# Optimization experiments

Hardware: AMD Instinct MI355X
Metric: run time of the kernel (lower is better)

The kernel has to match this reference:

```python
import jax, jax.numpy as jnp
import numpy as np

DIM = 1024
NUM_HEADS = 16
DPH = DIM // NUM_HEADS
B, S = 4, 2048
LN_EPS = 1e-5


def layer_norm(x, g, b):
    mu = jnp.mean(x, axis=-1, keepdims=True)
    var = jnp.mean((x - mu) ** 2, axis=-1, keepdims=True)
    return (x - mu) * jax.lax.rsqrt(var + LN_EPS) * g + b


def setup_inputs() -> dict:
    key = jax.random.key(0)
    ks = jax.random.split(key, 10)
    sd = 0.02
    return {
        "x": jax.random.normal(ks[0], (B, S, DIM), dtype=jnp.float32),
        "Wq": jax.random.normal(ks[1], (DIM, DIM), dtype=jnp.float32) * sd,
        "Wk": jax.random.normal(ks[2], (DIM, DIM), dtype=jnp.float32) * sd,
        "Wv": jax.random.normal(ks[3], (DIM, DIM), dtype=jnp.float32) * sd,
        "bq": jnp.zeros((DIM,), dtype=jnp.float32),
        "bk": jnp.zeros((DIM,), dtype=jnp.float32),
        "bv": jnp.zeros((DIM,), dtype=jnp.float32),
        "ln1_g": jnp.ones((DIM,), dtype=jnp.float32),
        "ln1_b": jnp.zeros((DIM,), dtype=jnp.float32),
        "W1": jax.random.normal(ks[4], (DIM, 4 * DIM), dtype=jnp.float32) * sd,
        "b1": jnp.zeros((4 * DIM,), dtype=jnp.float32),
        "W2": jax.random.normal(ks[5], (4 * DIM, DIM), dtype=jnp.float32) * sd,
        "b2": jnp.zeros((DIM,), dtype=jnp.float32),
        "ln2_g": jnp.ones((DIM,), dtype=jnp.float32),
        "ln2_b": jnp.zeros((DIM,), dtype=jnp.float32),
    }


def reference(x, Wq, Wk, Wv, bq, bk, bv, ln1_g, ln1_b, W1, b1, W2, b2, ln2_g, ln2_b):
    b, s, d = x.shape
    # QKV projections (heads are independent linears -> one fused GEMM each)
    q = (x @ Wq + bq).reshape(b, s, NUM_HEADS, DPH)
    k = (x @ Wk + bk).reshape(b, s, NUM_HEADS, DPH)
    v = (x @ Wv + bv).reshape(b, s, NUM_HEADS, DPH)
    # Faithful quirk: module scales by 1/sqrt(dph) twice => 1/dph total
    scores = jnp.einsum("bqhd,bkhd->bhqk", q, k) / DPH
    causal = jnp.tril(jnp.ones((s, s), dtype=bool))
    scores = jnp.where(causal, scores, -1e9)
    attn = jax.nn.softmax(scores, axis=-1)
    out_attn = jnp.einsum("bhqk,bkhd->bqhd", attn, v).reshape(b, s, d)
    # Add & Norm 1 (no output projection in original)
    h = layer_norm(out_attn + x, ln1_g, ln1_b)
    # Feed-forward (dropout is identity at eval)
    ffn = jax.nn.relu(h @ W1 + b1) @ W2 + b2
    # Add & Norm 2
    return layer_norm(ffn + h, ln2_g, ln2_b)
```

## Files before the change

### kernel.cpp

```cpp
#include <hip/hip_runtime.h>
#include <hip/hip_bf16.h>

typedef __bf16 bf16_t;
typedef __bf16 bf16x8 __attribute__((ext_vector_type(8)));
typedef __bf16 bf16x4 __attribute__((ext_vector_type(4)));
typedef float  floatx4 __attribute__((ext_vector_type(4)));

#define DIM    1024
#define S_LEN  2048
#define NHEAD  16

template <typename T>
__device__ __forceinline__ bf16x8 load8bf(const T* src) {
  if constexpr (sizeof(T) == 2) {
    return *reinterpret_cast<const bf16x8*>(src);
  } else {
    floatx4 f0 = *reinterpret_cast<const floatx4*>(src);
    floatx4 f1 = *reinterpret_cast<const floatx4*>(src + 4);
    bf16x8 h;
    h[0] = (bf16_t)f0[0]; h[1] = (bf16_t)f0[1];
    h[2] = (bf16_t)f0[2]; h[3] = (bf16_t)f0[3];
    h[4] = (bf16_t)f1[0]; h[5] = (bf16_t)f1[1];
    h[6] = (bf16_t)f1[2]; h[7] = (bf16_t)f1[3];
    return h;
  }
}

__device__ __forceinline__ void gll16(const bf16_t* g, bf16_t* l) {
  __builtin_amdgcn_global_load_lds(
      (const __attribute__((address_space(1))) void*)g,
      (__attribute__((address_space(3))) void*)l, 16, 0, 0);
}

__device__ __forceinline__ void xcd_remap(int& bx, int& by, int& bz) {
  const int gx = gridDim.x, gy = gridDim.y, gz = gridDim.z;
  const int nwg = gx * gy * gz;
  int lin = ((int)blockIdx.z * gy + blockIdx.y) * gx + blockIdx.x;
  int cid = lin;
  if ((nwg & 7) == 0) cid = (lin & 7) * (nwg >> 3) + (lin >> 3);
  bx = cid % gx;
  int t = cid / gx;
  bz = t % gz;
  by = t / gz;
}

__global__ __launch_bounds__(256) void conv_bf(const float* __restrict__ in,
                                               bf16_t* __restrict__ out) {
  size_t i = ((size_t)blockIdx.x * 256 + threadIdx.x) * 8;
  *reinterpret_cast<bf16x8*>(out + i) = load8bf(in + i);
}

__global__ __launch_bounds__(256) void convT3(
    const float* __restrict__ in0, int ldi0, bf16_t* __restrict__ out0,
    const float* __restrict__ in1, int ldi1, bf16_t* __restrict__ out1,
    const float* __restrict__ in2, int ldi2, bf16_t* __restrict__ out2,
    int ldo) {
  __shared__ bf16_t tile[32][33];
  const int z = blockIdx.z;
  const float* in = (z == 0) ? in0 : ((z == 1) ? in1 : in2);
  bf16_t* out = (z == 0) ? out0 : ((z == 1) ? out1 : out2);
  int ldi = (z == 0) ? ldi0 : ((z == 1) ? ldi1 : ldi2);
  int tx = threadIdx.x, ty = threadIdx.y;
  int n0 = blockIdx.x * 32, k0 = blockIdx.y * 32;
#pragma unroll
  for (int i = 0; i < 4; ++i)
    tile[ty + 8 * i][tx] = (bf16_t)in[(size_t)(k0 + ty + 8 * i) * ldi + n0 + tx];
  __syncthreads();
#pragma unroll
  for (int i = 0; i < 4; ++i)
    out[(size_t)(n0 + ty + 8 * i) * ldo + k0 + tx] = tile[tx][ty + 8 * i];
}

#define BM 128
#define BN 128
#define BK 32

template <typename TC>
__global__ __launch_bounds__(256) void gemm_abt(
    const bf16_t* __restrict__ A, int lda,
    const bf16_t* __restrict__ Bt, int zBRow,
    TC* __restrict__ C, int ldc, int zCOff,
    const float* __restrict__ bias0, const float* __restrict__ bias1,
    const float* __restrict__ bias2,
    int K, int relu, int accum) {
  __shared__ bf16_t As[2][BM * BK];
  __shared__ bf16_t Bs[2][BN * BK];

  int bx, by, bz;
  xcd_remap(bx, by, bz);
  const int z = bz;
  const float* bias = (z == 0) ? bias0 : ((z == 1) ? bias1 : bias2);
  const bf16_t* Bz = Bt + (size_t)z * zBRow * K;
  C += (size_t)z * zCOff;

  const int tid  = threadIdx.x;
  const int lane = tid & 63;
  const int wave = tid >> 6;
  const int wr   = wave >> 1;
  const int wc   = wave & 1;
  const int quad = lane >> 4;
  const int l15  = lane & 15;
  const int m0   = by * BM;
  const int n0   = bx * BN;
  const int swz = ((lane & 3) ^ ((lane >> 3) & 3)) * 8;
  const int rsw = (l15 >> 1) & 3;

  auto stageB = [&](int buf, int kt) {
#pragma unroll
    for (int i = 0; i < 2; ++i)
      gll16(Bz + (size_t)(n0 + wave * 32 + i * 16 + (lane >> 2)) * K +
                kt * BK + swz,
            &Bs[buf][(wave * 32 + i * 16) * BK]);
  };
  auto stageA = [&](int buf, int kt) {
#pragma unroll
    for (int i = 0; i < 2; ++i)
      gll16(A + (size_t)(m0 + wave * 32 + i * 16 + (lane >> 2)) * lda +
                kt * BK + swz,
            &As[buf][(wave * 32 + i * 16) * BK]);
  };

  floatx4 acc[4][4];
#pragma unroll
  for (int i = 0; i < 4; ++i)
#pragma unroll
    for (int j = 0; j < 4; ++j) acc[i][j] = (floatx4)(0.0f);

  const int kIters = K / BK;
  stageB(0, 0);
  stageA(0, 0);
  __syncthreads();

  int cur = 0;
  for (int kt = 0; kt < kIters; ++kt) {
    const int nxt = cur ^ 1;
    if (kt + 1 < kIters) {
      stageB(nxt, kt + 1);
      stageA(nxt, kt + 1);
    }

    bf16x8 a[4], b[4];
#pragma unroll
    for (int i = 0; i < 4; ++i)
      a[i] = *reinterpret_cast<const bf16x8*>(
          &As[cur][(wr * 64 + i * 16 + l15) * BK + (quad ^ rsw) * 8]);
#pragma unroll
    for (int j = 0; j < 4; ++j)
      b[j] = *reinterpret_cast<const bf16x8*>(
          &Bs[cur][(wc * 64 + j * 16 + l15) * BK + (quad ^ rsw) * 8]);
#pragma unroll
    for (int i = 0; i < 4; ++i)
#pragma unroll
      for (int j = 0; j < 4; ++j)
        acc[i][j] = __builtin_amdgcn_mfma_f32_16x16x32_bf16(a[i], b[j], acc[i][j], 0, 0, 0);

    __syncthreads();
    cur = nxt;
  }

#pragma unroll
  for (int j = 0; j < 4; ++j) {
    int gn = n0 + wc * 64 + j * 16 + l15;
    float bv = bias ? bias[gn] : 0.0f;
#pragma unroll
    for (int i = 0; i < 4; ++i) {
      int gm = m0 + wr * 64 + i * 16 + quad * 4;
#pragma unroll
      for (int r = 0; r < 4; ++r) {
        float v = acc[i][j][r] + bv;
        if (relu) v = fmaxf(v, 0.0f);
        size_t idx = (size_t)(gm + r) * ldc + gn;
        if (accum) v += (float)C[idx];
        C[idx] = (TC)v;
      }
    }
  }
}

__global__ __launch_bounds__(256) void transpose_v(const bf16_t* __restrict__ in,
                                                   bf16_t* __restrict__ outp) {
  __shared__ bf16_t tile[32][33];
  int tx = threadIdx.x, ty = threadIdx.y;
  int s0 = blockIdx.x * 32, d0 = blockIdx.y * 32, bh = blockIdx.z;
  int z = bh >> 4, h = bh & 15;
  const bf16_t* src = in + (size_t)z * S_LEN * 3072 + 2048 + h * 64;
#pragma unroll
  for (int i = 0; i < 4; ++i)
    tile[ty + 8 * i][tx] = src[(size_t)(s0 + ty + 8 * i) * 3072 + d0 + tx];
  __syncthreads();
  bf16_t* dst = outp + (size_t)bh * 64 * S_LEN;
#pragma unroll
  for (int i = 0; i < 4; ++i)
    dst[(size_t)(d0 + ty + 8 * i) * S_LEN + s0 + tx] = tile[tx][ty + 8 * i];
}

#define TQ  64
#define TK  64
#define AST 72
#define QSCALE 0.02254211f

struct KVregs { bf16x8 k[2]; bf16x8 v[2]; };

__global__ __launch_bounds__(256, 2) void attn_mfma2(
    const bf16_t* __restrict__ qkv, const bf16_t* __restrict__ vt,
    float* __restrict__ out) {
  __shared__ bf16_t QsPs[TQ * AST];
  __shared__ bf16_t Ks[TK * AST];
  __shared__ bf16_t Vs[TK * AST];

  const int tid  = threadIdx.x;
  const int lane = tid & 63;
  const int w    = tid >> 6;
  const int quad = lane >> 4;
  const int l15  = lane & 15;
  int pi, h, z;
  xcd_remap(pi, h, z);
  const int qb2[2] = {pi, 31 - pi};
  const bf16_t* qkv_b = qkv + (size_t)z * S_LEN * 3072;
  const bf16_t* vt_bh = vt + ((size_t)z * NHEAD + h) * 64 * S_LEN;
  float* out_b = out + (size_t)z * S_LEN * DIM;

  const int ktEnd = qb2[1] + 1;

  auto kv_load = [&](KVregs& r, int kt) {
#pragma unroll
    for (int p = 0; p < 2; ++p) {
      int id  = p * 256 + tid;
      int row = id >> 3;
      int c8  = (id & 7) * 8;
      r.k[p] = *reinterpret_cast<const bf16x8*>(
          qkv_b + (size_t)(kt * TK + row) * 3072 + 1024 + h * 64 + c8);
      r.v[p] = *reinterpret_cast<const bf16x8*>(
          vt_bh + (size_t)row * S_LEN + kt * TK + c8);
    }
  };
  auto kv_write = [&](KVregs& r) {
#pragma unroll
    for (int p = 0; p < 2; ++p) {
      int id  = p * 256 + tid;
      int row = id >> 3;
      int c8  = (id & 7) * 8;
      *reinterpret_cast<bf16x8*>(&Ks[row * AST + c8]) = r.k[p];
      *reinterpret_cast<bf16x8*>(&Vs[row * AST + c8]) = r.v[p];
    }
  };

  KVregs RA, RB;
  kv_load(RA, 0);

  bf16x8 aq[2][2];
  for (int tile = 0; tile < 2; ++tile) {
    if (tile) __syncthreads();
    const int qg0 = qb2[tile] * TQ;
#pragma unroll
    for (int p = 0; p < 2; ++p) {
      int id  = p * 256 + tid;
      int row = id >> 3;
      int c8  = (id & 7) * 8;
      bf16x8 v = *reinterpret_cast<const bf16x8*>(
          qkv_b + (size_t)(qg0 + row) * 3072 + h * 64 + c8);
      bf16x8 o;
#pragma unroll
      for (int e = 0; e < 8; ++e) o[e] = (bf16_t)((float)v[e] * QSCALE);
      *reinterpret_cast<bf16x8*>(&QsPs[row * AST + c8]) = o;
    }
    __syncthreads();
#pragma unroll
    for (int ks = 0; ks < 2; ++ks)
      aq[tile][ks] = *reinterpret_cast<const bf16x8*>(
          &QsPs[(w * 16 + l15) * AST + ks * 32 + quad * 8]);
  }

  float lp[2][4];
  floatx4 O[2][4];
#pragma unroll
  for (int t = 0; t < 2; ++t)
#pragma unroll
    for (int r = 0; r < 4; ++r) lp[t][r] = 0.0f;
#pragma unroll
  for (int t = 0; t < 2; ++t)
#pragma unroll
    for (int dt = 0; dt < 4; ++dt) O[t][dt] = (floatx4)(0.0f);

  auto step = [&](int kt, KVregs& cur, KVregs& nxt) {
    if (kt + 1 < ktEnd) kv_load(nxt, kt + 1);
    asm volatile("s_waitcnt lgkmcnt(0)" ::: "memory");
    __builtin_amdgcn_s_barrier();
    kv_write(cur);
    asm volatile("s_waitcnt lgkmcnt(0)" ::: "memory");
    __builtin_amdgcn_s_barrier();

    bf16x8 bk[4][2], bv[4][2];
#pragma unroll
    for (int i = 0; i < 4; ++i)
#pragma unroll
      for (int ks = 0; ks < 2; ++ks) {
        bk[i][ks] = *reinterpret_cast<const bf16x8*>(
            &Ks[(i * 16 + l15) * AST + ks * 32 + quad * 8]);
        bv[i][ks] = *reinterpret_cast<const bf16x8*>(
            &Vs[(i * 16 + l15) * AST + ks * 32 + quad * 8]);
      }

#pragma unroll
    for (int tile = 0; tile < 2; ++tile) {
      const int qtb = qb2[tile] * TQ + w * 16;
      if (kt * TK > qtb + 15) continue;

      floatx4 s[4];
      __builtin_amdgcn_s_setprio(1);
#pragma unroll
      for (int ktl = 0; ktl < 4; ++ktl) {
        s[ktl] = __builtin_amdgcn_mfma_f32_16x16x32_bf16(
            aq[tile][0], bk[ktl][0], (floatx4)(0.0f), 0, 0, 0);
        s[ktl] = __builtin_amdgcn_mfma_f32_16x16x32_bf16(
            aq[tile][1], bk[ktl][1], s[ktl], 0, 0, 0);
      }
      __builtin_amdgcn_s_setprio(0);
      if (kt * TK + TK - 1 > qtb) {
#pragma unroll
        for (int ktl = 0; ktl < 4; ++ktl) {
          int gk = kt * TK + ktl * 16 + l15;
#pragma unroll
          for (int r = 0; r < 4; ++r) {
            int gq = qtb + quad * 4 + r;
            if (gk > gq) s[ktl][r] = -1e30f;
          }
        }
      }
#pragma unroll
      for (int ktl = 0; ktl < 4; ++ktl)
#pragma unroll
        for (int r = 0; r < 4; ++r) {
          float p = exp2f(s[ktl][r]);
          lp[tile][r] += p;
          QsPs[(w * 16 + quad * 4 + r) * AST + ktl * 16 + l15] = (bf16_t)p;
        }

      bf16x8 ap0 = *reinterpret_cast<const bf16x8*>(
          &QsPs[(w * 16 + l15) * AST + quad * 8]);
      bf16x8 ap1 = *reinterpret_cast<const bf16x8*>(
          &QsPs[(w * 16 + l15) * AST + 32 + quad * 8]);
      __builtin_amdgcn_s_setprio(1);
#pragma unroll
      for (int dt = 0; dt < 4; ++dt) {
        O[tile][dt] = __builtin_amdgcn_mfma_f32_16x16x32_bf16(
            ap0, bv[dt][0], O[tile][dt], 0, 0, 0);
        O[tile][dt] = __builtin_amdgcn_mfma_f32_16x16x32_bf16(
            ap1, bv[dt][1], O[tile][dt], 0, 0, 0);
      }
      __builtin_amdgcn_s_setprio(0);
    }
  };

  for (int kt = 0; kt < ktEnd; kt += 2) {
    step(kt, RA, RB);
    if (kt + 1 < ktEnd) step(kt + 1, RB, RA);
  }

#pragma unroll
  for (int tile = 0; tile < 2; ++tile) {
    const int qg0 = qb2[tile] * TQ;
    float inv[4];
#pragma unroll
    for (int r = 0; r < 4; ++r) {
      float lv = lp[tile][r];
#pragma unroll
      for (int off = 1; off < 16; off <<= 1) lv += __shfl_xor(lv, off);
      inv[r] = 1.0f / lv;
    }
#pragma unroll
    for (int dt = 0; dt < 4; ++dt)
#pragma unroll
      for (int r = 0; r < 4; ++r)
        out_b[(size_t)(qg0 + w * 16 + quad * 4 + r) * DIM +
              h * 64 + dt * 16 + l15] = O[tile][dt][r] * inv[r];
  }
}

template <typename TA>
__global__ __launch_bounds__(256) void add_ln_k(const TA* a,
                                                const float* b,
                                                const float* __restrict__ g,
                                                const float* __restrict__ be,
                                                float* out,
                                                bf16_t* __restrict__ bfout) {
  const int row = blockIdx.x;
  const int t   = threadIdx.x;
  const size_t base = (size_t)row * DIM;

  float x[4];
  {
    floatx4 bv = *reinterpret_cast<const floatx4*>(b + base + t * 4);
    if (a) {
      if constexpr (sizeof(TA) == 2) {
        bf16x4 av = *reinterpret_cast<const bf16x4*>(a + base + t * 4);
#pragma unroll
        for (int i = 0; i < 4; ++i) x[i] = (float)av[i] + bv[i];
      } else {
        floatx4 av = *reinterpret_cast<const floatx4*>(a + base + t * 4);
#pragma unroll
        for (int i = 0; i < 4; ++i) x[i] = av[i] + bv[i];
      }
    } else {
#pragma unroll
      for (int i = 0; i < 4; ++i) x[i] = bv[i];
    }
  }
  float s1 = 0.0f, s2 = 0.0f;
#pragma unroll
  for (int i = 0; i < 4; ++i) { s1 += x[i]; s2 += x[i] * x[i]; }
#pragma unroll
  for (int off = 32; off; off >>= 1) {
    s1 += __shfl_xor(s1, off);
    s2 += __shfl_xor(s2, off);
  }
  __shared__ float ls1[4], ls2[4];
  if ((t & 63) == 0) { ls1[t >> 6] = s1; ls2[t >> 6] = s2; }
  __syncthreads();
  float S1 = ls1[0] + ls1[1] + ls1[2] + ls1[3];
  float S2 = ls2[0] + ls2[1] + ls2[2] + ls2[3];
  float mu  = S1 * (1.0f / DIM);
  float var = S2 * (1.0f / DIM) - mu * mu;
  float rs  = rsqrtf(var + 1e-5f);
#pragma unroll
  for (int i = 0; i < 4; ++i) {
    int c = t * 4 + i;
    float hv = (x[i] - mu) * rs * g[c] + be[c];
    out[base + c] = hv;
    if (bfout) bfout[base + c] = (bf16_t)hv;
  }
}

extern "C" void kernel_launch(void* const* d_in, const int* in_sizes, int n_in,
                              void* d_out, int out_size, void* d_ws, size_t ws_size,
                              hipStream_t stream) {
  const float* x   = (const float*)d_in[0];
  const float* Wq  = (const float*)d_in[1];
  const float* Wk  = (const float*)d_in[2];
  const float* Wv  = (const float*)d_in[3];
  const float* bq  = (const float*)d_in[4];
  const float* bk  = (const float*)d_in[5];
  const float* bv  = (const float*)d_in[6];
  const float* g1  = (const float*)d_in[7];
  const float* be1 = (const float*)d_in[8];
  const float* W1  = (const float*)d_in[9];
  const float* b1  = (const float*)d_in[10];
  const float* W2  = (const float*)d_in[11];
  const float* b2  = (const float*)d_in[12];
  const float* g2  = (const float*)d_in[13];
  const float* be2 = (const float*)d_in[14];
  float* out = (float*)d_out;
  char*  ws  = (char*)d_ws;

  bf16_t* WqkvT = (bf16_t*)(ws);
  bf16_t* qkv2  = (bf16_t*)(ws + 6291456);
  bf16_t* vt    = (bf16_t*)(ws + 31457280);
  bf16_t* xbf   = (bf16_t*)(ws + 31457280);
  bf16_t* W1Tq  = (bf16_t*)(ws);
  bf16_t* W2Tq  = (bf16_t*)(ws + 2097152);
  bf16_t* hbf   = (bf16_t*)(ws + 4194304);
  bf16_t* mid   = (bf16_t*)(ws + 20971520);

  dim3 tb(32, 8);
  convT3<<<dim3(32, 32, 3), tb, 0, stream>>>(
      Wq, 1024, WqkvT, Wk, 1024, WqkvT + 1048576, Wv, 1024, WqkvT + 2097152, 1024);

  for (int p = 0; p < 2; ++p) {
    const float* xp   = x   + (size_t)p * 2 * S_LEN * DIM;
    float*       outp = out + (size_t)p * 2 * S_LEN * DIM;
    conv_bf<<<2048, 256, 0, stream>>>(xp, xbf);
    gemm_abt<bf16_t><<<dim3(8, 32, 3), 256, 0, stream>>>(
        xbf, 1024, WqkvT, 1024, qkv2, 3072, 1024, bq, bk, bv, 1024, 0, 0);
    transpose_v<<<dim3(64, 2, 32), tb, 0, stream>>>(qkv2, vt);
    attn_mfma2<<<dim3(16, 16, 2), 256, 0, stream>>>(qkv2, vt, outp);
  }
  add_ln_k<float><<<8192, 256, 0, stream>>>(out, x, g1, be1, out, hbf);

  for (int q = 0; q < 4; ++q) {
    convT3<<<dim3(32, 32, 2), tb, 0, stream>>>(
        W1 + q * 1024, 4096, W1Tq,
        W2 + (size_t)q * 1024 * 1024, 1024, W2Tq,
        nullptr, 0, nullptr, 1024);
    gemm_abt<bf16_t><<<dim3(8, 64, 1), 256, 0, stream>>>(
        hbf, 1024, W1Tq, 0, mid, 1024, 0, b1 + q * 1024, nullptr, nullptr,
        1024, 1, 0);
    gemm_abt<float><<<dim3(8, 64, 1), 256, 0, stream>>>(
        mid, 1024, W2Tq, 0, out, 1024, 0, (q == 0) ? b2 : nullptr, nullptr,
        nullptr, 1024, 0, 1);
  }
  add_ln_k<float><<<8192, 256, 0, stream>>>(nullptr, out, g2, be2, out, nullptr);
}
```

Baseline: 666.6 us.

## Triple-buffer GEMM shared tiles with vmcnt-based waits and single barrier per iteration

Switches the GEMM main loop from double to triple buffering of the A/B shared-memory tiles. Loads are prefetched two iterations ahead, and each iteration waits only on older loads via s_waitcnt vmcnt(4) before a single raw barrier, replacing the two __syncthreads per step. This aims to hide more global-load latency and cut synchronization cost. In exchange it uses half again as much LDS, which can lower occupancy, and correctness depends on the hand-counted number of outstanding loads.

```diff
diff --git a/kernel.cpp b/kernel.cpp
--- a/kernel.cpp
+++ b/kernel.cpp
@@ -73,7 +73,7 @@
 
 #define BM 128
 #define BN 128
-#define BK 32
+#define BK32 32
 
 template <typename TC>
 __global__ __launch_bounds__(256) void gemm_abt(
@@ -83,8 +83,8 @@
     const float* __restrict__ bias0, const float* __restrict__ bias1,
     const float* __restrict__ bias2,
     int K, int relu, int accum) {
-  __shared__ bf16_t As[2][BM * BK];
-  __shared__ bf16_t Bs[2][BN * BK];
+  __shared__ bf16_t As[3][BM * BK32];
+  __shared__ bf16_t Bs[3][BN * BK32];
 
   int bx, by, bz;
   xcd_remap(bx, by, bz);
@@ -105,19 +105,17 @@
   const int swz = ((lane & 3) ^ ((lane >> 3) & 3)) * 8;
   const int rsw = (l15 >> 1) & 3;
 
-  auto stageB = [&](int buf, int kt) {
+  auto stage = [&](int buf, int kt) {
 #pragma unroll
     for (int i = 0; i < 2; ++i)
       gll16(Bz + (size_t)(n0 + wave * 32 + i * 16 + (lane >> 2)) * K +
-                kt * BK + swz,
-            &Bs[buf][(wave * 32 + i * 16) * BK]);
-  };
-  auto stageA = [&](int buf, int kt) {
+                kt * BK32 + swz,
+            &Bs[buf][(wave * 32 + i * 16) * BK32]);
 #pragma unroll
     for (int i = 0; i < 2; ++i)
       gll16(A + (size_t)(m0 + wave * 32 + i * 16 + (lane >> 2)) * lda +
-                kt * BK + swz,
-            &As[buf][(wave * 32 + i * 16) * BK]);
+                kt * BK32 + swz,
+            &As[buf][(wave * 32 + i * 16) * BK32]);
   };
 
   floatx4 acc[4][4];
@@ -126,36 +124,34 @@
 #pragma unroll
     for (int j = 0; j < 4; ++j) acc[i][j] = (floatx4)(0.0f);
 
-  const int kIters = K / BK;
-  stageB(0, 0);
-  stageA(0, 0);
-  __syncthreads();
-
-  int cur = 0;
+  const int kIters = K / BK32;
+  stage(0, 0);
+  stage(1, 1);
+
+  int cur = 0, sbuf = 2;
   for (int kt = 0; kt < kIters; ++kt) {
-    const int nxt = cur ^ 1;
-    if (kt + 1 < kIters) {
-      stageB(nxt, kt + 1);
-      stageA(nxt, kt + 1);
-    }
+    if (kt + 1 < kIters) asm volatile("s_waitcnt vmcnt(4)" ::: "memory");
+    else                 asm volatile("s_waitcnt vmcnt(0)" ::: "memory");
+    __builtin_amdgcn_s_barrier();
+    if (kt + 2 < kIters) stage(sbuf, kt + 2);
 
     bf16x8 a[4], b[4];
 #pragma unroll
     for (int i = 0; i < 4; ++i)
       a[i] = *reinterpret_cast<const bf16x8*>(
-          &As[cur][(wr * 64 + i * 16 + l15) * BK + (quad ^ rsw) * 8]);
+          &As[cur][(wr * 64 + i * 16 + l15) * BK32 + (quad ^ rsw) * 8]);
 #pragma unroll
     for (int j = 0; j < 4; ++j)
       b[j] = *reinterpret_cast<const bf16x8*>(
-          &Bs[cur][(wc * 64 + j * 16 + l15) * BK + (quad ^ rsw) * 8]);
+          &Bs[cur][(wc * 64 + j * 16 + l15) * BK32 + (quad ^ rsw) * 8]);
 #pragma unroll
     for (int i = 0; i < 4; ++i)
 #pragma unroll
       for (int j = 0; j < 4; ++j)
         acc[i][j] = __builtin_amdgcn_mfma_f32_16x16x32_bf16(a[i], b[j], acc[i][j], 0, 0, 0);
 
-    __syncthreads();
-    cur = nxt;
+    cur = (cur == 2) ? 0 : cur + 1;
+    sbuf = (sbuf == 2) ? 0 : sbuf + 1;
   }
 
 #pragma unroll
```

After: 665.7 us. About the same (-0.1%).
